# Optimization experiments

Measured on AMD Instinct MI355X. Metric: run time of the kernel, lower is better.

The kernel has to match this reference:

```python
import jax, jax.numpy as jnp
import numpy as np

C = 128            # in_channels
B, H, W = 4, 256, 256
WS = 8             # window_size
N = WS * WS        # tokens per window
HIDDEN = int(N ** 0.5) * 2   # WindowScoreBias hidden_dim = 16
NUM_HEADS = 2


def setup_inputs() -> dict:
    key = jax.random.key(0)
    ks = jax.random.split(key, 8)
    # deterministic relative-position table (mirrors _gen_window_score_bias_input, reduction=1)
    coords = np.stack(np.meshgrid(np.arange(WS), np.arange(WS), indexing='ij'), axis=2).reshape(N, 2)
    delta = (coords[:, None, :] - coords[None, :, :]).reshape(N * N, 2)
    uniq, index = np.unique(delta, axis=0, return_inverse=True)  # lexsorted unique == sorted tuples
    uniq = uniq.astype(np.float32) / np.abs(uniq).max()
    return {
        'x': jax.random.normal(ks[0], (B, C, H, W), jnp.float32),
        'delta': jnp.asarray(uniq),                       # [U, 2]
        'index': jnp.asarray(index.astype(np.int32)),     # [N*N]
        'w_qkv': jax.random.normal(ks[1], (3 * C, C), jnp.float32) * 0.02,
        'b_qkv': jnp.zeros((3 * C,), jnp.float32),
        'w_head': jax.random.normal(ks[2], (C, C), jnp.float32) * 0.02,
        'b_head': jnp.zeros((C,), jnp.float32),
        'w_b1': jax.random.normal(ks[3], (HIDDEN, 2), jnp.float32) * 0.02,
        'b_b1': jnp.zeros((HIDDEN,), jnp.float32),
        'w_b2': jax.random.normal(ks[4], (1, HIDDEN), jnp.float32) * 0.02,
        'b_b2': jnp.zeros((1,), jnp.float32),
        'w_c1': jax.random.normal(ks[5], (C, C, 1, 1), jnp.float32) * (2.0 / C) ** 0.5,
        'b_c1': jnp.zeros((C,), jnp.float32),
        'w_c2': jax.random.normal(ks[6], (C, C, 3, 3), jnp.float32) * (2.0 / (9 * C)) ** 0.5,
        'b_c2': jnp.zeros((C,), jnp.float32),
    }


def _conv(x, w, b):
    y = jax.lax.conv_general_dilated(x, w, (1, 1), 'VALID',
                                     dimension_numbers=('NCHW', 'OIHW', 'NCHW'))
    return y + b[None, :, None, None]


def reference(x, delta, index, w_qkv, b_qkv, w_head, b_head,
              w_b1, b_b1, w_b2, b_b2, w_c1, b_c1, w_c2, b_c2):
    Bx, Cx, Hx, Wx = x.shape
    oh, ow = Hx // WS, Wx // WS
    dk = Cx // NUM_HEADS
    # WindowScoreBias: MLP over unique deltas, gather by index -> [N, N]
    hmlp = jax.nn.gelu(delta @ w_b1.T + b_b1, approximate=False)
    bias = (hmlp @ w_b2.T + b_b2)[index].reshape(N, N)
    # window partition: BCHW -> (B*oh*ow, N, C)
    xw = x.reshape(Bx, Cx, oh, WS, ow, WS).transpose(0, 2, 4, 3, 5, 1).reshape(Bx * oh * ow, N, Cx)
    qkv = xw @ w_qkv.T + b_qkv
    q, k, v = jnp.split(qkv, 3, axis=-1)
    heads = lambda t: t.reshape(-1, N, NUM_HEADS, dk).transpose(0, 2, 1, 3)  # [Bw,h,N,dk]
    q, k, v = heads(q), heads(k), heads(v)
    scores = jnp.einsum('bhnd,bhmd->bhnm', q, k) * (1.0 / float(np.sqrt(dk))) + bias
    attn = jax.nn.softmax(scores, axis=-1)
    o = jnp.einsum('bhnm,bhmd->bhnd', attn, v)
    o = o.transpose(0, 2, 1, 3).reshape(-1, N, Cx) @ w_head.T + b_head
    # window reverse: (B*oh*ow, N, C) -> BCHW
    o = o.reshape(Bx, oh, ow, WS, WS, Cx).transpose(0, 5, 1, 3, 2, 4).reshape(Bx, Cx, Hx, Wx)
    x = x + o
    # conv_mlp: 1x1 conv -> GELU -> replication pad -> 3x3 conv -> LeakyReLU(0.1)
    y = jax.nn.gelu(_conv(x, w_c1, b_c1), approximate=False)
    y = jnp.pad(y, ((0, 0), (0, 0), (1, 1), (1, 1)), mode='edge')
    y = _conv(y, w_c2, b_c2)
    y = jnp.where(y > 0, y, 0.1 * y)
    return x + y
```

## Files before the change

### kernel.cpp

```cpp
#include <hip/hip_runtime.h>

typedef short v8s __attribute__((ext_vector_type(8)));
typedef float v4f __attribute__((ext_vector_type(4)));
typedef unsigned short v4u __attribute__((ext_vector_type(4)));

#define MFMA(a,b,c) __builtin_amdgcn_mfma_f32_16x16x32_bf16((a),(b),(c),0,0,0)

__device__ __forceinline__ unsigned short f2b(float f) {
  unsigned int x = __builtin_bit_cast(unsigned int, f);
  x += 0x7fffu + ((x >> 16) & 1u);
  return (unsigned short)(x >> 16);
}

__device__ __forceinline__ float b2f(unsigned short u) {
  unsigned int x = ((unsigned int)u) << 16;
  return __builtin_bit_cast(float, x);
}

__device__ __forceinline__ float gelu_exact(float v) {
  return 0.5f * v * (1.0f + erff(v * 0.70710678118654752f));
}

__device__ __forceinline__ float gelu_fast(float v) {
  float u = 1.5957691f * v * (1.0f + 0.044715f * v * v);
  return v * (1.0f / (1.0f + __expf(-u)));
}

__global__ void prep_kernel(const float* __restrict__ wqkv, const float* __restrict__ whead,
                            const float* __restrict__ wc1, const float* __restrict__ wc2,
                            const float* __restrict__ delta, const int* __restrict__ indexv,
                            const float* __restrict__ wb1, const float* __restrict__ bb1,
                            const float* __restrict__ wb2, const float* __restrict__ bb2,
                            unsigned short* __restrict__ wqkv_b, unsigned short* __restrict__ whead_b,
                            unsigned short* __restrict__ wc1_b, unsigned short* __restrict__ w2r_b,
                            float* __restrict__ bias_ws) {
  int i = blockIdx.x * 256 + threadIdx.x;
  if (i < 49152) { wqkv_b[i] = f2b(wqkv[i]); return; }
  i -= 49152;
  if (i < 16384) { whead_b[i] = f2b(whead[i]); return; }
  i -= 16384;
  if (i < 16384) { wc1_b[i] = f2b(wc1[i]); return; }
  i -= 16384;
  if (i < 147456) {
    int o = i / 1152; int rem = i - o * 1152; int pos = rem >> 7; int c = rem & 127;
    w2r_b[i] = f2b(wc2[o * 1152 + c * 9 + pos]);
    return;
  }
  i -= 147456;
  if (i < 4096) {
    int u = indexv[i];
    float d0 = delta[2 * u], d1 = delta[2 * u + 1];
    float acc = bb2[0];
    #pragma unroll
    for (int j = 0; j < 16; ++j) {
      float t = d0 * wb1[2 * j] + d1 * wb1[2 * j + 1] + bb1[j];
      acc += gelu_exact(t) * wb2[j];
    }
    bias_ws[i] = acc;
  }
}

__global__ __launch_bounds__(256, 2) void xt_kernel(
    const float* __restrict__ x, unsigned short* __restrict__ t16) {
  __shared__ unsigned short T[256 * 129];
  const int tid = threadIdx.x;
  const int bid = blockIdx.x;
  const int b = bid >> 8, h = bid & 255;
  const float* src = x + (size_t)b * 128 * 65536 + h * 256;

  #pragma unroll
  for (int it = 0; it < 32; ++it) {
    int u = it * 256 + tid;
    int c = u >> 6, w4 = u & 63;
    float4 v = *(const float4*)(src + (size_t)c * 65536 + w4 * 4);
    int base = (w4 * 4) * 129 + c;
    T[base]       = f2b(v.x);
    T[base + 129] = f2b(v.y);
    T[base + 258] = f2b(v.z);
    T[base + 387] = f2b(v.w);
  }
  __syncthreads();

  unsigned short* dst = t16 + (size_t)((b * 256 + h) * 256) * 128;
  #pragma unroll
  for (int it = 0; it < 16; ++it) {
    int idx = it * 256 + tid;
    int px = idx >> 4, c8 = idx & 15;
    const unsigned short* t = &T[px * 129 + c8 * 8];
    v8s o;
    #pragma unroll
    for (int j = 0; j < 8; ++j) o[j] = (short)t[j];
    *(v8s*)(dst + px * 128 + c8 * 8) = o;
  }
}

__global__ __launch_bounds__(256, 3) void attn_kernel(
    const float* __restrict__ bias,
    const unsigned short* __restrict__ wqkv_b, const unsigned short* __restrict__ whead_b,
    const float* __restrict__ bqkv, const float* __restrict__ bhead,
    unsigned short* __restrict__ t16) {
  __shared__ unsigned short U0[128 * 72];
  __shared__ unsigned short QP[64 * 136];
  __shared__ unsigned short KO[64 * 136];
  unsigned short* const XS = U0;
  unsigned short* const VT = U0;

  const int tid = threadIdx.x;
  const int wv = tid >> 6, lane = tid & 63, quad = lane >> 4, l15 = lane & 15;
  const int bid0 = blockIdx.x;
  const int bid = ((bid0 & 7) << 9) | (bid0 >> 3);
  const int bb = bid >> 10, rem = bid & 1023;
  const int h0 = (rem >> 5) * 8, w0 = (rem & 31) * 8;

  #pragma unroll
  for (int it = 0; it < 4; ++it) {
    int idx = it * 256 + tid;
    int token = idx >> 4, c8 = idx & 15;
    int py = token >> 3, px = token & 7;
    *(v8s*)(&XS[token * 136 + c8 * 8]) =
        *(const v8s*)(t16 + (size_t)((bb * 256 + h0 + py) * 256 + w0 + px) * 128 + c8 * 8);
  }
  __syncthreads();

  v4u vpk[2][4];
  #pragma unroll
  for (int part = 0; part < 3; ++part) {
    v4f acc[2][4] = {};
    #pragma unroll
    for (int ks = 0; ks < 4; ++ks) {
      v8s afr[2];
      #pragma unroll
      for (int i = 0; i < 2; ++i)
        afr[i] = *(const v8s*)(wqkv_b + (size_t)(part * 128 + (2 * wv + i) * 16 + l15) * 128 + ks * 32 + quad * 8);
      v8s bfr[4];
      #pragma unroll
      for (int ct = 0; ct < 4; ++ct)
        bfr[ct] = *(const v8s*)(&XS[(ct * 16 + l15) * 136 + ks * 32 + quad * 8]);
      #pragma unroll
      for (int i = 0; i < 2; ++i)
        #pragma unroll
        for (int ct = 0; ct < 4; ++ct)
          acc[i][ct] = MFMA(afr[i], bfr[ct], acc[i][ct]);
    }
    #pragma unroll
    for (int i = 0; i < 2; ++i) {
      int ol0 = (2 * wv + i) * 16 + quad * 4;
      float4 bq = *(const float4*)(bqkv + part * 128 + ol0);
      float bqa[4] = {bq.x, bq.y, bq.z, bq.w};
      #pragma unroll
      for (int ct = 0; ct < 4; ++ct) {
        int token = ct * 16 + l15;
        v4u pk = {f2b(acc[i][ct][0] + bqa[0]), f2b(acc[i][ct][1] + bqa[1]),
                  f2b(acc[i][ct][2] + bqa[2]), f2b(acc[i][ct][3] + bqa[3])};
        if (part == 0)      *(v4u*)(&QP[token * 136 + ol0]) = pk;
        else if (part == 1) *(v4u*)(&KO[token * 136 + ol0]) = pk;
        else                vpk[i][ct] = pk;
      }
    }
  }
  __syncthreads();

  #pragma unroll
  for (int i = 0; i < 2; ++i) {
    int ol0 = (2 * wv + i) * 16 + quad * 4;
    #pragma unroll
    for (int ct = 0; ct < 4; ++ct) {
      int token = ct * 16 + l15;
      VT[(ol0 + 0) * 72 + token] = vpk[i][ct][0];
      VT[(ol0 + 1) * 72 + token] = vpk[i][ct][1];
      VT[(ol0 + 2) * 72 + token] = vpk[i][ct][2];
      VT[(ol0 + 3) * 72 + token] = vpk[i][ct][3];
    }
  }

  const int t0 = wv * 16;
  v4f sc[2][4] = {};
  #pragma unroll
  for (int h = 0; h < 2; ++h)
    #pragma unroll
    for (int ks = 0; ks < 2; ++ks) {
      v8s afr = *(const v8s*)(&QP[(t0 + l15) * 136 + h * 64 + ks * 32 + quad * 8]);
      #pragma unroll
      for (int ct = 0; ct < 4; ++ct) {
        v8s bfr = *(const v8s*)(&KO[(ct * 16 + l15) * 136 + h * 64 + ks * 32 + quad * 8]);
        sc[h][ct] = MFMA(afr, bfr, sc[h][ct]);
      }
    }
  float linv[2][4];
  const int rowbase = (t0 + quad * 4) * 64 + l15;
  #pragma unroll
  for (int h = 0; h < 2; ++h) {
    float sv[4][4];
    #pragma unroll
    for (int ct = 0; ct < 4; ++ct)
      #pragma unroll
      for (int r = 0; r < 4; ++r)
        sv[ct][r] = sc[h][ct][r] * 0.125f + bias[rowbase + r * 64 + ct * 16];
    #pragma unroll
    for (int r = 0; r < 4; ++r) {
      float m = fmaxf(fmaxf(sv[0][r], sv[1][r]), fmaxf(sv[2][r], sv[3][r]));
      m = fmaxf(m, __shfl_xor(m, 1, 16));
      m = fmaxf(m, __shfl_xor(m, 2, 16));
      m = fmaxf(m, __shfl_xor(m, 4, 16));
      m = fmaxf(m, __shfl_xor(m, 8, 16));
      float s = 0.f;
      #pragma unroll
      for (int ct = 0; ct < 4; ++ct) { float p = __expf(sv[ct][r] - m); sv[ct][r] = p; s += p; }
      s += __shfl_xor(s, 1, 16);
      s += __shfl_xor(s, 2, 16);
      s += __shfl_xor(s, 4, 16);
      s += __shfl_xor(s, 8, 16);
      linv[h][r] = 1.0f / s;
    }
    #pragma unroll
    for (int ct = 0; ct < 4; ++ct)
      #pragma unroll
      for (int r = 0; r < 4; ++r)
        QP[(t0 + quad * 4 + r) * 136 + h * 64 + ct * 16 + l15] = f2b(sv[ct][r]);
  }
  __syncthreads();

  v4f ov[2][4] = {};
  #pragma unroll
  for (int h = 0; h < 2; ++h)
    #pragma unroll
    for (int ks = 0; ks < 2; ++ks) {
      v8s afr = *(const v8s*)(&QP[(t0 + l15) * 136 + h * 64 + ks * 32 + quad * 8]);
      #pragma unroll
      for (int ct = 0; ct < 4; ++ct) {
        v8s bfr = *(const v8s*)(&VT[(h * 64 + ct * 16 + l15) * 72 + ks * 32 + quad * 8]);
        ov[h][ct] = MFMA(afr, bfr, ov[h][ct]);
      }
    }
  #pragma unroll
  for (int h = 0; h < 2; ++h)
    #pragma unroll
    for (int ct = 0; ct < 4; ++ct)
      #pragma unroll
      for (int r = 0; r < 4; ++r)
        KO[(t0 + quad * 4 + r) * 136 + h * 64 + ct * 16 + l15] = f2b(ov[h][ct][r] * linv[h][r]);
  __syncthreads();

  v4f pj[8] = {};
  #pragma unroll
  for (int ks = 0; ks < 4; ++ks) {
    v8s afr = *(const v8s*)(&KO[(t0 + l15) * 136 + ks * 32 + quad * 8]);
    #pragma unroll
    for (int ct = 0; ct < 8; ++ct) {
      v8s bfr = *(const v8s*)(whead_b + (size_t)(ct * 16 + l15) * 128 + ks * 32 + quad * 8);
      pj[ct] = MFMA(afr, bfr, pj[ct]);
    }
  }
  {
    int token0 = t0 + quad * 4;
    int py = token0 >> 3, px = token0 & 7;
    const unsigned short* xtw = t16 + (size_t)((bb * 256 + h0 + py) * 256 + w0 + px) * 128;
    #pragma unroll
    for (int ct = 0; ct < 8; ++ct) {
      int o = ct * 16 + l15;
      float bh = bhead[o];
      #pragma unroll
      for (int r = 0; r < 4; ++r) {
        float xa = b2f(xtw[(size_t)r * 128 + o]);
        XS[(token0 + r) * 136 + o] = f2b(xa + pj[ct][r] + bh);
      }
    }
  }
  __syncthreads();

  #pragma unroll
  for (int it = 0; it < 4; ++it) {
    int idx = it * 256 + tid;
    int token = idx >> 4, c8 = idx & 15;
    int py = token >> 3, px = token & 7;
    *(v8s*)(t16 + (size_t)((bb * 256 + h0 + py) * 256 + w0 + px) * 128 + c8 * 8) =
        *(const v8s*)(&XS[token * 136 + c8 * 8]);
  }
}

__global__ __launch_bounds__(256, 3) void conv2_kernel(
    const unsigned short* __restrict__ w2r, const unsigned short* __restrict__ wc1_b,
    const unsigned short* __restrict__ t16,
    const float* __restrict__ bc1, const float* __restrict__ bc2, float* __restrict__ xo) {
  __shared__ unsigned short XH[144 * 136];
  unsigned short* const YH = XH;
  const int tid = threadIdx.x;
  const int wv = tid >> 6, lane = tid & 63, quad = lane >> 4, l15 = lane & 15;
  const int bid0 = blockIdx.x;
  const int bid = ((bid0 & 7) << 9) | (bid0 >> 3);
  const int bb = bid >> 10, rem = bid & 1023;
  const int y0 = (rem >> 3) * 2, x0 = (rem & 7) * 32;

  v4u xpre[2][4];
  #pragma unroll
  for (int i = 0; i < 2; ++i) {
    int o0 = (2 * wv + i) * 16 + quad * 4;
    #pragma unroll
    for (int ct = 0; ct < 4; ++ct) {
      int pix = ct * 16 + l15, typ = pix >> 5, txp = pix & 31;
      xpre[i][ct] = *(const v4u*)(t16 + (size_t)((bb * 256 + y0 + typ) * 256 + x0 + txp) * 128 + o0);
    }
  }

  for (int it = 0; it < 9; ++it) {
    int idx = it * 256 + tid;
    if (idx < 2176) {
      int hp = idx >> 4, c8 = idx & 15;
      int iy = hp / 34, ix = hp - iy * 34;
      int hy = y0 - 1 + iy; hy = hy < 0 ? 0 : (hy > 255 ? 255 : hy);
      int hx = x0 - 1 + ix; hx = hx < 0 ? 0 : (hx > 255 ? 255 : hx);
      *(v8s*)(&XH[hp * 136 + c8 * 8]) =
          *(const v8s*)(t16 + (size_t)((bb * 256 + hy) * 256 + hx) * 128 + c8 * 8);
    }
  }
  __syncthreads();

  v4f yacc[2][9] = {};
  #pragma unroll
  for (int ks = 0; ks < 4; ++ks) {
    v8s afr[2];
    #pragma unroll
    for (int i = 0; i < 2; ++i)
      afr[i] = *(const v8s*)(wc1_b + (size_t)((2 * wv + i) * 16 + l15) * 128 + ks * 32 + quad * 8);
    v8s bfr[9];
    #pragma unroll
    for (int ct = 0; ct < 9; ++ct)
      bfr[ct] = *(const v8s*)(&XH[(ct * 16 + l15) * 136 + ks * 32 + quad * 8]);
    #pragma unroll
    for (int i = 0; i < 2; ++i)
      #pragma unroll
      for (int ct = 0; ct < 9; ++ct)
        yacc[i][ct] = MFMA(afr[i], bfr[ct], yacc[i][ct]);
  }
  __syncthreads();

  #pragma unroll
  for (int i = 0; i < 2; ++i) {
    int ol0 = (2 * wv + i) * 16 + quad * 4;
    float4 bq = *(const float4*)(bc1 + ol0);
    float bqa[4] = {bq.x, bq.y, bq.z, bq.w};
    #pragma unroll
    for (int ct = 0; ct < 9; ++ct) {
      int token = ct * 16 + l15;
      v4u pk = {f2b(gelu_fast(yacc[i][ct][0] + bqa[0])),
                f2b(gelu_fast(yacc[i][ct][1] + bqa[1])),
                f2b(gelu_fast(yacc[i][ct][2] + bqa[2])),
                f2b(gelu_fast(yacc[i][ct][3] + bqa[3]))};
      *(v4u*)(&YH[token * 136 + ol0]) = pk;
    }
  }
  __syncthreads();

  v4f acc[2][4] = {};
  int bct[4];
  #pragma unroll
  for (int ct = 0; ct < 4; ++ct) {
    int pix = ct * 16 + l15, typ = pix >> 5, txp = pix & 31;
    bct[ct] = (typ * 34 + txp) * 136 + quad * 8;
  }
  const unsigned short* wb0 = w2r + (size_t)((2 * wv + 0) * 16 + l15) * 1152 + quad * 8;
  const unsigned short* wb1 = w2r + (size_t)((2 * wv + 1) * 16 + l15) * 1152 + quad * 8;
  #pragma unroll
  for (int ks = 0; ks < 36; ++ks) {
    const int pos = ks >> 2, cb = ks & 3;
    const int ky = pos / 3, kx = pos - ky * 3;
    const int koff = (ky * 34 + kx) * 136 + cb * 32;
    v8s a0 = *(const v8s*)(wb0 + ks * 32);
    v8s a1 = *(const v8s*)(wb1 + ks * 32);
    #pragma unroll
    for (int ct = 0; ct < 4; ++ct) {
      v8s bfr = *(const v8s*)(&YH[bct[ct] + koff]);
      acc[0][ct] = MFMA(a0, bfr, acc[0][ct]);
      acc[1][ct] = MFMA(a1, bfr, acc[1][ct]);
    }
  }

  #pragma unroll
  for (int i = 0; i < 2; ++i) {
    int o0 = (2 * wv + i) * 16 + quad * 4;
    float4 bc = *(const float4*)(bc2 + o0);
    float bca[4] = {bc.x, bc.y, bc.z, bc.w};
    #pragma unroll
    for (int ct = 0; ct < 4; ++ct) {
      int pix = ct * 16 + l15, typ = pix >> 5, txp = pix & 31;
      float* po = xo + (size_t)(bb * 128 + o0) * 65536 + (y0 + typ) * 256 + (x0 + txp);
      #pragma unroll
      for (int r = 0; r < 4; ++r) {
        float v = acc[i][ct][r] + bca[r];
        v = v > 0.f ? v : 0.1f * v;
        po[(size_t)r * 65536] = v + b2f(xpre[i][ct][r]);
      }
    }
  }
}

extern "C" void kernel_launch(void* const* d_in, const int* in_sizes, int n_in,
                              void* d_out, int out_size, void* d_ws, size_t ws_size,
                              hipStream_t stream) {
  (void)in_sizes; (void)n_in; (void)out_size; (void)ws_size;
  const float* x      = (const float*)d_in[0];
  const float* delta  = (const float*)d_in[1];
  const int*   indexv = (const int*)d_in[2];
  const float* w_qkv  = (const float*)d_in[3];
  const float* b_qkv  = (const float*)d_in[4];
  const float* w_head = (const float*)d_in[5];
  const float* b_head = (const float*)d_in[6];
  const float* w_b1   = (const float*)d_in[7];
  const float* b_b1   = (const float*)d_in[8];
  const float* w_b2   = (const float*)d_in[9];
  const float* b_b2   = (const float*)d_in[10];
  const float* w_c1   = (const float*)d_in[11];
  const float* b_c1   = (const float*)d_in[12];
  const float* w_c2   = (const float*)d_in[13];
  const float* b_c2   = (const float*)d_in[14];
  float* out = (float*)d_out;

  char* ws = (char*)d_ws;
  float*          bias_ws = (float*)(ws + 0);
  unsigned short* wqkv_b  = (unsigned short*)(ws + 16384);
  unsigned short* whead_b = (unsigned short*)(ws + 114688);
  unsigned short* wc1_b   = (unsigned short*)(ws + 147456);
  unsigned short* w2r_b   = (unsigned short*)(ws + 180224);
  unsigned short* t16     = (unsigned short*)(ws + 475136 + 67108864);

  prep_kernel<<<912, 256, 0, stream>>>(w_qkv, w_head, w_c1, w_c2, delta, indexv,
                                       w_b1, b_b1, w_b2, b_b2,
                                       wqkv_b, whead_b, wc1_b, w2r_b, bias_ws);
  xt_kernel<<<1024, 256, 0, stream>>>(x, t16);
  attn_kernel<<<4096, 256, 0, stream>>>(bias_ws, wqkv_b, whead_b,
                                        b_qkv, b_head, t16);
  conv2_kernel<<<4096, 256, 0, stream>>>(w2r_b, wc1_b, t16, b_c1, b_c2, out);
}
```

Measured before the change: 572.6 us.

## Split transpose kernel per half-row, cache residual in registers, use packed bf16 converts

The transpose kernel now handles half a row per block, with half the LDS and twice as many blocks, so more blocks can be resident per CU. The attention kernel copies the residual input from LDS into registers before XS is overwritten, so it no longer re-reads it from global memory in the epilogue. Several float-to-bf16 conversions now use the hardware v_cvt_pk_bf16_f32 instruction in place of the manual rounding sequence. Keeping 32 residual values live in registers through the attention body may raise register pressure.

```diff
diff --git a/kernel.cpp b/kernel.cpp
--- a/kernel.cpp
+++ b/kernel.cpp
@@ -15,6 +15,12 @@
 __device__ __forceinline__ float b2f(unsigned short u) {
   unsigned int x = ((unsigned int)u) << 16;
   return __builtin_bit_cast(float, x);
+}
+
+__device__ __forceinline__ unsigned int cvtpk(float lo, float hi) {
+  unsigned int r;
+  asm("v_cvt_pk_bf16_f32 %0, %1, %2" : "=v"(r) : "v"(lo), "v"(hi));
+  return r;
 }
 
 __device__ __forceinline__ float gelu_exact(float v) {
@@ -60,18 +66,18 @@
   }
 }
 
-__global__ __launch_bounds__(256, 2) void xt_kernel(
+__global__ __launch_bounds__(256, 4) void xt_kernel(
     const float* __restrict__ x, unsigned short* __restrict__ t16) {
-  __shared__ unsigned short T[256 * 129];
+  __shared__ unsigned short T[128 * 129];
   const int tid = threadIdx.x;
   const int bid = blockIdx.x;
-  const int b = bid >> 8, h = bid & 255;
-  const float* src = x + (size_t)b * 128 * 65536 + h * 256;
-
-  #pragma unroll
-  for (int it = 0; it < 32; ++it) {
+  const int b = bid >> 9, h = (bid >> 1) & 255, xh = (bid & 1) * 128;
+  const float* src = x + (size_t)b * 128 * 65536 + h * 256 + xh;
+
+  #pragma unroll
+  for (int it = 0; it < 16; ++it) {
     int u = it * 256 + tid;
-    int c = u >> 6, w4 = u & 63;
+    int c = u >> 5, w4 = u & 31;
     float4 v = *(const float4*)(src + (size_t)c * 65536 + w4 * 4);
     int base = (w4 * 4) * 129 + c;
     T[base]       = f2b(v.x);
@@ -81,9 +87,9 @@
   }
   __syncthreads();
 
-  unsigned short* dst = t16 + (size_t)((b * 256 + h) * 256) * 128;
-  #pragma unroll
-  for (int it = 0; it < 16; ++it) {
+  unsigned short* dst = t16 + (size_t)((b * 256 + h) * 256 + xh) * 128;
+  #pragma unroll
+  for (int it = 0; it < 8; ++it) {
     int idx = it * 256 + tid;
     int px = idx >> 4, c8 = idx & 15;
     const unsigned short* t = &T[px * 129 + c8 * 8];
@@ -122,6 +128,7 @@
   }
   __syncthreads();
 
+  const int t0 = wv * 16;
   v4u vpk[2][4];
   #pragma unroll
   for (int part = 0; part < 3; ++part) {
@@ -150,12 +157,29 @@
       #pragma unroll
       for (int ct = 0; ct < 4; ++ct) {
         int token = ct * 16 + l15;
-        v4u pk = {f2b(acc[i][ct][0] + bqa[0]), f2b(acc[i][ct][1] + bqa[1]),
-                  f2b(acc[i][ct][2] + bqa[2]), f2b(acc[i][ct][3] + bqa[3])};
-        if (part == 0)      *(v4u*)(&QP[token * 136 + ol0]) = pk;
-        else if (part == 1) *(v4u*)(&KO[token * 136 + ol0]) = pk;
-        else                vpk[i][ct] = pk;
+        if (part < 2) {
+          uint2 pk2;
+          pk2.x = cvtpk(acc[i][ct][0] + bqa[0], acc[i][ct][1] + bqa[1]);
+          pk2.y = cvtpk(acc[i][ct][2] + bqa[2], acc[i][ct][3] + bqa[3]);
+          if (part == 0) *(uint2*)(&QP[token * 136 + ol0]) = pk2;
+          else           *(uint2*)(&KO[token * 136 + ol0]) = pk2;
+        } else {
+          v4u pk = {f2b(acc[i][ct][0] + bqa[0]), f2b(acc[i][ct][1] + bqa[1]),
+                    f2b(acc[i][ct][2] + bqa[2]), f2b(acc[i][ct][3] + bqa[3])};
+          vpk[i][ct] = pk;
+        }
       }
+    }
+  }
+
+  unsigned short xres[8][4];
+  {
+    int token0 = t0 + quad * 4;
+    #pragma unroll
+    for (int ct = 0; ct < 8; ++ct) {
+      int o = ct * 16 + l15;
+      #pragma unroll
+      for (int r = 0; r < 4; ++r) xres[ct][r] = XS[(token0 + r) * 136 + o];
     }
   }
   __syncthreads();
@@ -173,7 +197,6 @@
     }
   }
 
-  const int t0 = wv * 16;
   v4f sc[2][4] = {};
   #pragma unroll
   for (int h = 0; h < 2; ++h)
@@ -253,17 +276,13 @@
   }
   {
     int token0 = t0 + quad * 4;
-    int py = token0 >> 3, px = token0 & 7;
-    const unsigned short* xtw = t16 + (size_t)((bb * 256 + h0 + py) * 256 + w0 + px) * 128;
     #pragma unroll
     for (int ct = 0; ct < 8; ++ct) {
       int o = ct * 16 + l15;
       float bh = bhead[o];
       #pragma unroll
-      for (int r = 0; r < 4; ++r) {
-        float xa = b2f(xtw[(size_t)r * 128 + o]);
-        XS[(token0 + r) * 136 + o] = f2b(xa + pj[ct][r] + bh);
-      }
+      for (int r = 0; r < 4; ++r)
+        XS[(token0 + r) * 136 + o] = f2b(b2f(xres[ct][r]) + pj[ct][r] + bh);
     }
   }
   __syncthreads();
@@ -342,11 +361,10 @@
     #pragma unroll
     for (int ct = 0; ct < 9; ++ct) {
       int token = ct * 16 + l15;
-      v4u pk = {f2b(gelu_fast(yacc[i][ct][0] + bqa[0])),
-                f2b(gelu_fast(yacc[i][ct][1] + bqa[1])),
-                f2b(gelu_fast(yacc[i][ct][2] + bqa[2])),
-                f2b(gelu_fast(yacc[i][ct][3] + bqa[3]))};
-      *(v4u*)(&YH[token * 136 + ol0]) = pk;
+      uint2 pk2;
+      pk2.x = cvtpk(gelu_fast(yacc[i][ct][0] + bqa[0]), gelu_fast(yacc[i][ct][1] + bqa[1]));
+      pk2.y = cvtpk(gelu_fast(yacc[i][ct][2] + bqa[2]), gelu_fast(yacc[i][ct][3] + bqa[3]));
+      *(uint2*)(&YH[token * 136 + ol0]) = pk2;
     }
   }
   __syncthreads();
@@ -426,7 +444,7 @@
   prep_kernel<<<912, 256, 0, stream>>>(w_qkv, w_head, w_c1, w_c2, delta, indexv,
                                        w_b1, b_b1, w_b2, b_b2,
                                        wqkv_b, whead_b, wc1_b, w2r_b, bias_ws);
-  xt_kernel<<<1024, 256, 0, stream>>>(x, t16);
+  xt_kernel<<<2048, 256, 0, stream>>>(x, t16);
   attn_kernel<<<4096, 256, 0, stream>>>(bias_ws, wqkv_b, whead_b,
                                         b_qkv, b_head, t16);
   conv2_kernel<<<4096, 256, 0, stream>>>(w2r_b, wc1_b, t16, b_c1, b_c2, out);
```

Measured after the change: 572.3 us. About the same (-0.0%).
